# Optimization experiments

Measured on AMD Instinct MI355X. Metric: run time of the kernel, lower is better.

The kernel has to match this reference:

```python
import jax, jax.numpy as jnp
import numpy as np

HEADS = 4
SCALE = 10.0
DIM = 128
VOL = (16, 16, 16)
BATCH = 2
EPS = 1e-12  # F.normalize eps


def setup_inputs() -> dict:
    key = jax.random.key(0)
    ks = jax.random.split(key, 7)
    h, w, z = VOL
    shape = (BATCH, DIM, h, w, z)
    wstd = 1.0 / np.sqrt(DIM)
    return {
        "x": jax.random.normal(ks[0], shape, dtype=jnp.float32),
        "cond_x": jax.random.normal(ks[1], shape, dtype=jnp.float32),
        "Wq": jax.random.normal(ks[2], (DIM, DIM), dtype=jnp.float32) * wstd,
        "bq": jnp.zeros((DIM,), dtype=jnp.float32),
        "Wk": jax.random.normal(ks[3], (DIM, DIM), dtype=jnp.float32) * wstd,
        "bk": jnp.zeros((DIM,), dtype=jnp.float32),
        "Wv": jax.random.normal(ks[4], (DIM, DIM), dtype=jnp.float32) * wstd,
        "bv": jnp.zeros((DIM,), dtype=jnp.float32),
        "Wo": jax.random.normal(ks[5], (DIM, DIM), dtype=jnp.float32) * wstd,
        "bo": jnp.zeros((DIM,), dtype=jnp.float32),
    }


def _l2norm_last(t):
    # F.normalize(t, dim=-1): divide by max(||t||_2, eps) along last axis
    n = jnp.sqrt(jnp.sum(t * t, axis=-1, keepdims=True))
    return t / jnp.maximum(n, EPS)


def reference(x, cond_x, Wq, bq, Wk, bk, Wv, bv, Wo, bo):
    b, c, h, w, z = x.shape
    N = h * w * z
    d = c // HEADS
    xf = x.reshape(b, c, N)          # conv1x1 == per-voxel linear over channels
    cf = cond_x.reshape(b, c, N)
    q = jnp.einsum('oc,bcn->bon', Wq, xf) + bq[None, :, None]
    k = jnp.einsum('oc,bcn->bon', Wk, cf) + bk[None, :, None]
    v = jnp.einsum('oc,bcn->bon', Wv, cf) + bv[None, :, None]
    # 'b (h c) n -> b h c n'
    q = q.reshape(b, HEADS, d, N)
    k = k.reshape(b, HEADS, d, N)
    v = v.reshape(b, HEADS, d, N)
    # NOTE: original normalizes dim=-1 of [b,h,d,N] -> over the SPATIAL axis
    q = _l2norm_last(q)
    k = _l2norm_last(k)
    sim = jnp.einsum('bhdi,bhdj->bhij', q, k) * SCALE   # [b,h,N,N]
    attn = jax.nn.softmax(sim, axis=-1)
    out = jnp.einsum('bhij,bhdj->bhid', attn, v)        # [b,h,N,d]
    # 'b h n d -> b (h d) n' then back to volume
    out = out.transpose(0, 1, 3, 2).reshape(b, c, N)
    out = jnp.einsum('oc,bcn->bon', Wo, out) + bo[None, :, None]
    return out.reshape(b, c, h, w, z)
```

## Files before the change

kernel.cpp:

```cpp
#include <hip/hip_runtime.h>
#include <hip/hip_bf16.h>
#include <math.h>

#define NSP 4096
#define CD 128
#define NB 2
#define NH 4
#define JS 4
#define JSTEP 64
#define NSTEP ((NSP / JS) / JSTEP)

typedef __attribute__((ext_vector_type(8))) short bf16x8;
typedef __attribute__((ext_vector_type(4))) float f32x4;

static constexpr float QSCALE = 10.0f * 1.4426950408889634f;

__device__ __forceinline__ ushort f2bf(float f) {
    union { float f; unsigned u; } v; v.f = f;
    unsigned r = v.u + 0x7fffu + ((v.u >> 16) & 1u);
    return (ushort)(r >> 16);
}
__device__ __forceinline__ float bf2f(ushort u) {
    union { unsigned u; float f; } v; v.u = ((unsigned)u) << 16;
    return v.f;
}
__device__ __forceinline__ unsigned pk2bf(float a, float b) {
    union { __hip_bfloat162 h; unsigned u; } t;
    t.h = __float22bfloat162_rn(make_float2(a, b));
    return t.u;
}
__device__ __forceinline__ void gload_lds16(const void* g, void* l) {
    __builtin_amdgcn_global_load_lds(
        (const __attribute__((address_space(1))) unsigned int*)g,
        (__attribute__((address_space(3))) unsigned int*)l, 16, 0, 0);
}

__global__ __launch_bounds__(256) void cast_all(
    const float* __restrict__ x, const float* __restrict__ cx,
    const float* __restrict__ Wq, const float* __restrict__ Wk,
    const float* __restrict__ Wv, const float* __restrict__ Wo,
    ushort* __restrict__ Xt, ushort* __restrict__ Ct, ushort* __restrict__ Wall)
{
    const int t = threadIdx.x;
    if (blockIdx.x >= 128) {
        const int sub = blockIdx.x - 128;
        const int m = blockIdx.z * 2 + blockIdx.y;
        const float* src = (m == 0) ? Wq : (m == 1) ? Wk : (m == 2) ? Wv : Wo;
        const int off = sub * 1024 + t * 4;
        const float4 v = *(const float4*)(src + off);
        ushort4 o;
        o.x = f2bf(v.x); o.y = f2bf(v.y); o.z = f2bf(v.z); o.w = f2bf(v.w);
        *(ushort4*)(Wall + m * 16384 + off) = o;
        return;
    }
    __shared__ ushort L[32][130];
    const int n0 = blockIdx.x * 32;
    const int b  = blockIdx.y;
    const float* in = (blockIdx.z == 0) ? x : cx;
    ushort* outp    = (blockIdx.z == 0) ? Xt : Ct;
    const int nl = t & 31, cq = t >> 5;
    #pragma unroll
    for (int cc = cq; cc < CD; cc += 8)
        L[nl][cc] = f2bf(in[((size_t)b * CD + cc) * NSP + n0 + nl]);
    __syncthreads();
    const int nr = t >> 3, cs = (t & 7) * 16;
    unsigned u[8];
    #pragma unroll
    for (int w = 0; w < 8; ++w)
        u[w] = (unsigned)L[nr][cs + 2 * w] | ((unsigned)L[nr][cs + 2 * w + 1] << 16);
    ushort* dst = outp + ((size_t)(b * NSP + n0 + nr)) * CD + cs;
    *(uint4*)(dst)     = make_uint4(u[0], u[1], u[2], u[3]);
    *(uint4*)(dst + 8) = make_uint4(u[4], u[5], u[6], u[7]);
}

__global__ __launch_bounds__(256) void proj_qkv_mfma(
    const ushort* __restrict__ Xt, const ushort* __restrict__ Ct,
    const ushort* __restrict__ Wall,
    const float* __restrict__ Bq, const float* __restrict__ Bk, const float* __restrict__ Bv,
    ushort* __restrict__ Qt, ushort* __restrict__ Kt, ushort* __restrict__ V16,
    float* __restrict__ partQ, float* __restrict__ partK)
{
    const int t = threadIdx.x;
    const int wid = t >> 6, lane = t & 63;
    const int g = lane >> 4, n16 = lane & 15;
    const int nt = blockIdx.x;
    const int b  = nt >> 8;
    const int xblk = nt & 255;
    const int nb = xblk * 16;

    const size_t xrow = ((size_t)(b * NSP + nb + n16)) * CD;
    bf16x8 bx[4], bc[4];
    #pragma unroll
    for (int ks = 0; ks < 4; ++ks) {
        bx[ks] = *(const bf16x8*)(Xt + xrow + ks * 32 + g * 8);
        bc[ks] = *(const bf16x8*)(Ct + xrow + ks * 32 + g * 8);
    }
    const int jb = nb >> 6, jr = (nb & 63) + n16;

    #pragma unroll
    for (int hf = 0; hf < 2; ++hf) {
        const int o0 = hf * 64 + wid * 16;
        const ushort* Wq = Wall          + (size_t)(o0 + n16) * CD;
        const ushort* Wk = Wall + 16384  + (size_t)(o0 + n16) * CD;
        const ushort* Wv = Wall + 32768  + (size_t)(o0 + n16) * CD;

        f32x4 aq = {0,0,0,0}, ak = {0,0,0,0}, av = {0,0,0,0};
        #pragma unroll
        for (int ks = 0; ks < 4; ++ks) {
            const int k0 = ks * 32 + g * 8;
            const bf16x8 wqf = *(const bf16x8*)(Wq + k0);
            const bf16x8 wkf = *(const bf16x8*)(Wk + k0);
            const bf16x8 wvf = *(const bf16x8*)(Wv + k0);
            aq = __builtin_amdgcn_mfma_f32_16x16x32_bf16(wqf, bx[ks], aq, 0, 0, 0);
            ak = __builtin_amdgcn_mfma_f32_16x16x32_bf16(wkf, bc[ks], ak, 0, 0, 0);
            av = __builtin_amdgcn_mfma_f32_16x16x32_bf16(wvf, bc[ks], av, 0, 0, 0);
        }
        float qv[4], kv[4], sq[4], sk[4];
        #pragma unroll
        for (int r = 0; r < 4; ++r) {
            const int o = o0 + 4 * g + r;
            qv[r] = aq[r] + Bq[o];
            kv[r] = ak[r] + Bk[o];
            V16[((size_t)(b * CD + o)) * NSP + nb + n16] = f2bf(av[r] + Bv[o]);
            sq[r] = qv[r] * qv[r]; sk[r] = kv[r] * kv[r];
        }
        {
            const int o_first = o0 + 4 * g;
            const int bh = b * NH + (o_first >> 5);
            const int chunk = ((o_first & 31) >> 3);
            const size_t idx = (((size_t)(bh * 64 + jb)) * 4 + chunk) * 512
                             + (size_t)jr * 8 + 4 * (g & 1);
            uint2 qs, ks2;
            qs.x  = pk2bf(qv[0], qv[1]); qs.y  = pk2bf(qv[2], qv[3]);
            ks2.x = pk2bf(kv[0], kv[1]); ks2.y = pk2bf(kv[2], kv[3]);
            *(uint2*)(Qt + idx) = qs;
            *(uint2*)(Kt + idx) = ks2;
        }
        #pragma unroll
        for (int r = 0; r < 4; ++r) {
            #pragma unroll
            for (int off = 1; off < 16; off <<= 1) {
                sq[r] += __shfl_xor(sq[r], off);
                sk[r] += __shfl_xor(sk[r], off);
            }
        }
        if (n16 == 0) {
            #pragma unroll
            for (int r = 0; r < 4; ++r) {
                const int ch = b * CD + o0 + 4 * g + r;
                partQ[(size_t)ch * 256 + xblk] = sq[r];
                partK[(size_t)ch * 256 + xblk] = sk[r];
            }
        }
    }
}

__global__ __launch_bounds__(256) void normfin(
    const float* __restrict__ partQ, const float* __restrict__ partK,
    float* __restrict__ fsc)
{
    const int ch = blockIdx.x;
    const int t = threadIdx.x;
    float vq = partQ[(size_t)ch * 256 + t];
    float vk = partK[(size_t)ch * 256 + t];
    #pragma unroll
    for (int off = 32; off > 0; off >>= 1) {
        vq += __shfl_down(vq, off, 64);
        vk += __shfl_down(vk, off, 64);
    }
    __shared__ float redq[4], redk[4];
    if ((t & 63) == 0) { redq[t >> 6] = vq; redk[t >> 6] = vk; }
    __syncthreads();
    if (t == 0) {
        const float nq = sqrtf(redq[0] + redq[1] + redq[2] + redq[3]);
        const float nk = sqrtf(redk[0] + redk[1] + redk[2] + redk[3]);
        fsc[ch] = QSCALE / (fmaxf(nq, 1e-12f) * fmaxf(nk, 1e-12f));
    }
}

__global__ __launch_bounds__(256, 4) void attn_mfma(
    const ushort* __restrict__ Qt, const ushort* __restrict__ Kt,
    const ushort* __restrict__ V16, const float* __restrict__ fsc,
    unsigned* __restrict__ pacc, float* __restrict__ pl)
{
    __shared__ __align__(16) ushort Kl[4][2048];
    __shared__ __align__(16) ushort Vl[4][2048];

    const int t = threadIdx.x;
    const int wid = t >> 6, lane = t & 63;
    const int g = lane >> 4, n16 = lane & 15;
    const int f = blockIdx.x;
    const int bh = f & 7, it32 = (f >> 3) & 31, js = f >> 8;
    const int b = bh >> 2, h = bh & 3;
    const int i0 = it32 * 128 + wid * 32;

    const ushort* QtB = Qt + (size_t)bh * NSP * 32;
    const ushort* KtB = Kt + (size_t)bh * NSP * 32;
    const ushort* Vb  = V16 + (size_t)(b * CD + h * 32) * NSP;

    const float* fb = fsc + b * CD + h * 32 + g * 8;
    const f32x4 fA = *(const f32x4*)(fb);
    const f32x4 fB = *(const f32x4*)(fb + 4);

    const size_t qoff = ((size_t)(i0 >> 6) * 4 + g) * 512 + (size_t)(i0 & 63) * 8;
    const bf16x8 qr0 = *(const bf16x8*)(QtB + qoff + n16 * 8);
    const bf16x8 qr1 = *(const bf16x8*)(QtB + qoff + (16 + n16) * 8);
    auto scaleq = [&](bf16x8 q) -> bf16x8 {
        union { unsigned u[4]; bf16x8 v; } o;
        o.u[0] = pk2bf(bf2f((ushort)q[0]) * fA.x, bf2f((ushort)q[1]) * fA.y);
        o.u[1] = pk2bf(bf2f((ushort)q[2]) * fA.z, bf2f((ushort)q[3]) * fA.w);
        o.u[2] = pk2bf(bf2f((ushort)q[4]) * fB.x, bf2f((ushort)q[5]) * fB.y);
        o.u[3] = pk2bf(bf2f((ushort)q[6]) * fB.z, bf2f((ushort)q[7]) * fB.w);
        return o.v;
    };
    const bf16x8 qf[2] = { scaleq(qr0), scaleq(qr1) };

    f32x4 acc[2][2] = {{{0,0,0,0},{0,0,0,0}},{{0,0,0,0},{0,0,0,0}}};
    float l0 = 0.f, l1 = 0.f;
    const f32x4 zero = {0,0,0,0};

    const int klp = lane ^ (wid * 2);
    const int vd  = wid * 8 + (lane >> 3);
    const int vsw = (lane & 7) ^ (lane >> 3);
    auto stageK = [&](int buf, int jt) {
        gload_lds16(KtB + ((size_t)(jt >> 6) * 4 + wid) * 512 + klp * 8,
                    &Kl[buf][wid * 512]);
    };
    auto stageV = [&](int buf, int jt) {
        gload_lds16(Vb + (size_t)vd * NSP + jt + vsw * 8, &Vl[buf][wid * 512]);
    };

    const int jbeg = js * (NSP / JS);
    stageK(0, jbeg);          stageV(0, jbeg);
    stageK(1, jbeg + JSTEP);  stageV(1, jbeg + JSTEP);

    for (int step = 0; step < NSTEP; ++step) {
        const int jt = jbeg + step * JSTEP;
        if (step + 2 < NSTEP) {
            stageK((step + 2) & 3, jt + 2 * JSTEP);
            stageV((step + 2) & 3, jt + 2 * JSTEP);
            asm volatile("s_waitcnt vmcnt(4)" ::: "memory");
        } else if (step + 1 < NSTEP) {
            asm volatile("s_waitcnt vmcnt(2)" ::: "memory");
        } else {
            asm volatile("s_waitcnt vmcnt(0)" ::: "memory");
        }
        __builtin_amdgcn_s_barrier();
        const int cur = step & 3;
        __builtin_amdgcn_s_setprio(1);

        bf16x8 kf[2][2];
        union { uint2 u2[2]; bf16x8 v; } vf[2][2];
        #pragma unroll
        for (int s = 0; s < 2; ++s) {
            kf[s][0] = *(const bf16x8*)(&Kl[cur][g * 512 + ((s * 32 + n16) ^ (g * 2)) * 8]);
            kf[s][1] = *(const bf16x8*)(&Kl[cur][g * 512 + ((s * 32 + 16 + n16) ^ (g * 2)) * 8]);
            const int c0 = ((4 * s + (g >> 1)) ^ (n16 & 7)) * 8 + (g & 1) * 4;
            const int c1 = ((4 * s + 2 + (g >> 1)) ^ (n16 & 7)) * 8 + (g & 1) * 4;
            vf[s][0].u2[0] = *(const uint2*)(&Vl[cur][n16 * 64 + c0]);
            vf[s][0].u2[1] = *(const uint2*)(&Vl[cur][n16 * 64 + c1]);
            vf[s][1].u2[0] = *(const uint2*)(&Vl[cur][(16 + n16) * 64 + c0]);
            vf[s][1].u2[1] = *(const uint2*)(&Vl[cur][(16 + n16) * 64 + c1]);
        }
        f32x4 sv[2][2][2];
        #pragma unroll
        for (int s = 0; s < 2; ++s)
            #pragma unroll
            for (int it = 0; it < 2; ++it) {
                sv[s][it][0] = __builtin_amdgcn_mfma_f32_16x16x32_bf16(kf[s][0], qf[it], zero, 0, 0, 0);
                sv[s][it][1] = __builtin_amdgcn_mfma_f32_16x16x32_bf16(kf[s][1], qf[it], zero, 0, 0, 0);
            }

        union { unsigned u[4]; bf16x8 v; } pf[2][2];
        #pragma unroll
        for (int s = 0; s < 2; ++s)
            #pragma unroll
            for (int it = 0; it < 2; ++it) {
                const f32x4 s0 = sv[s][it][0], s1 = sv[s][it][1];
                const float p0 = __builtin_amdgcn_exp2f(s0.x);
                const float p1 = __builtin_amdgcn_exp2f(s0.y);
                const float p2 = __builtin_amdgcn_exp2f(s0.z);
                const float p3 = __builtin_amdgcn_exp2f(s0.w);
                const float p4 = __builtin_amdgcn_exp2f(s1.x);
                const float p5 = __builtin_amdgcn_exp2f(s1.y);
                const float p6 = __builtin_amdgcn_exp2f(s1.z);
                const float p7 = __builtin_amdgcn_exp2f(s1.w);
                const float ps = ((p0 + p1) + (p2 + p3)) + ((p4 + p5) + (p6 + p7));
                if (it) l1 += ps; else l0 += ps;
                pf[s][it].u[0] = pk2bf(p0, p1);
                pf[s][it].u[1] = pk2bf(p2, p3);
                pf[s][it].u[2] = pk2bf(p4, p5);
                pf[s][it].u[3] = pk2bf(p6, p7);
            }

        #pragma unroll
        for (int s = 0; s < 2; ++s)
            #pragma unroll
            for (int it = 0; it < 2; ++it) {
                acc[it][0] = __builtin_amdgcn_mfma_f32_16x16x32_bf16(vf[s][0].v, pf[s][it].v, acc[it][0], 0, 0, 0);
                acc[it][1] = __builtin_amdgcn_mfma_f32_16x16x32_bf16(vf[s][1].v, pf[s][it].v, acc[it][1], 0, 0, 0);
            }
        __builtin_amdgcn_s_setprio(0);
    }

    l0 += __shfl_xor(l0, 16); l0 += __shfl_xor(l0, 32);
    l1 += __shfl_xor(l1, 16); l1 += __shfl_xor(l1, 32);

    const size_t base = (size_t)js * 8 + bh;
    if (lane < 16) {
        pl[base * NSP + i0 + n16]      = l0;
        pl[base * NSP + i0 + 16 + n16] = l1;
    }
    unsigned* pb = pacc + base * 16 * NSP;
    const int col0 = i0 + n16, col1 = i0 + 16 + n16;
    pb[(size_t)(2 * g)     * NSP + col0] = pk2bf(acc[0][0][0], acc[0][0][1]);
    pb[(size_t)(2 * g + 1) * NSP + col0] = pk2bf(acc[0][0][2], acc[0][0][3]);
    pb[(size_t)(8 + 2 * g)     * NSP + col0] = pk2bf(acc[0][1][0], acc[0][1][1]);
    pb[(size_t)(8 + 2 * g + 1) * NSP + col0] = pk2bf(acc[0][1][2], acc[0][1][3]);
    pb[(size_t)(2 * g)     * NSP + col1] = pk2bf(acc[1][0][0], acc[1][0][1]);
    pb[(size_t)(2 * g + 1) * NSP + col1] = pk2bf(acc[1][0][2], acc[1][0][3]);
    pb[(size_t)(8 + 2 * g)     * NSP + col1] = pk2bf(acc[1][1][0], acc[1][1][1]);
    pb[(size_t)(8 + 2 * g + 1) * NSP + col1] = pk2bf(acc[1][1][2], acc[1][1][3]);
}

__global__ __launch_bounds__(256) void combine_proj_out(
    const unsigned* __restrict__ pacc, const float* __restrict__ pl,
    const ushort* __restrict__ Wall, const float* __restrict__ Bo,
    float* __restrict__ outp)
{
    __shared__ __align__(16) ushort Yl[16][128];
    const int t = threadIdx.x;
    const int nt = blockIdx.x;
    const int b  = nt >> 8;
    const int nb = (nt & 255) * 16;

    {
        const int nl = t & 15, hh = (t >> 4) & 3, q = t >> 6;
        const int bh = b * NH + hh;
        const int n = nb + nl;
        float L = 0.f;
        #pragma unroll
        for (int s = 0; s < JS; ++s) L += pl[((size_t)(s * 8 + bh)) * NSP + n];
        const float invL = 1.0f / L;
        unsigned u[4];
        #pragma unroll
        for (int e = 0; e < 4; ++e) {
            const int dp = q * 4 + e;
            float a0 = 0.f, a1 = 0.f;
            #pragma unroll
            for (int s = 0; s < JS; ++s) {
                const unsigned w = pacc[(((size_t)(s * 8 + bh)) * 16 + dp) * NSP + n];
                union { unsigned u; float f; } lo, hi;
                lo.u = w << 16; hi.u = w & 0xffff0000u;
                a0 += lo.f; a1 += hi.f;
            }
            u[e] = pk2bf(a0 * invL, a1 * invL);
        }
        const int chunk = hh * 4 + q;
        *(uint4*)(&Yl[nl][((chunk ^ (nl & 7)) * 8)]) = make_uint4(u[0], u[1], u[2], u[3]);
    }
    __syncthreads();

    const int wid = t >> 6, lane = t & 63;
    const int g = lane >> 4, n16 = lane & 15;
    const ushort* Wo = Wall + 49152;
    #pragma unroll
    for (int half = 0; half < 2; ++half) {
        const int o0 = half * 64 + wid * 16;
        const size_t wrow = (size_t)(o0 + n16) * CD;
        f32x4 a = {0,0,0,0};
        #pragma unroll
        for (int ks = 0; ks < 4; ++ks) {
            const bf16x8 wf = *(const bf16x8*)(Wo + wrow + ks * 32 + g * 8);
            const int chunk = ks * 4 + g;
            const bf16x8 yf = *(const bf16x8*)(&Yl[n16][((chunk ^ (n16 & 7)) * 8)]);
            a = __builtin_amdgcn_mfma_f32_16x16x32_bf16(wf, yf, a, 0, 0, 0);
        }
        #pragma unroll
        for (int r = 0; r < 4; ++r) {
            const int o = o0 + 4 * g + r;
            outp[((size_t)(b * CD + o)) * NSP + nb + n16] = a[r] + Bo[o];
        }
    }
}

extern "C" void kernel_launch(void* const* d_in, const int* in_sizes, int n_in,
                              void* d_out, int out_size, void* d_ws, size_t ws_size,
                              hipStream_t stream)
{
    const float* x  = (const float*)d_in[0];
    const float* cx = (const float*)d_in[1];
    const float* Wq = (const float*)d_in[2];
    const float* bq = (const float*)d_in[3];
    const float* Wk = (const float*)d_in[4];
    const float* bk = (const float*)d_in[5];
    const float* Wv = (const float*)d_in[6];
    const float* bv = (const float*)d_in[7];
    const float* Wo = (const float*)d_in[8];
    const float* bo = (const float*)d_in[9];
    float* out = (float*)d_out;

    char* w = (char*)d_ws;
    float*   fsc  = (float*)w;   w += 4096;
    float*   partQ = (float*)w;  w += (size_t)NB * CD * 256 * 4;
    float*   partK = (float*)w;  w += (size_t)NB * CD * 256 * 4;
    ushort*  Qt   = (ushort*)w;  w += (size_t)NB * NH * NSP * 32 * 2;
    ushort*  Kt   = (ushort*)w;  w += (size_t)NB * NH * NSP * 32 * 2;
    ushort*  V16  = (ushort*)w;  w += (size_t)NB * CD * NSP * 2;
    unsigned* pacc = (unsigned*)w; w += (size_t)JS * 8 * 16 * NSP * 4;
    float*   pl   = (float*)w;   w += (size_t)JS * 8 * NSP * 4;
    ushort*  Xt   = (ushort*)w;  w += (size_t)NB * NSP * CD * 2;
    ushort*  Ct   = (ushort*)w;  w += (size_t)NB * NSP * CD * 2;
    ushort*  Wall = (ushort*)w;

    cast_all<<<dim3(144, NB, 2), 256, 0, stream>>>(x, cx, Wq, Wk, Wv, Wo, Xt, Ct, Wall);
    proj_qkv_mfma<<<dim3(512), 256, 0, stream>>>(Xt, Ct, Wall, bq, bk, bv,
                                                 Qt, Kt, V16, partQ, partK);
    normfin<<<dim3(256), 256, 0, stream>>>(partQ, partK, fsc);
    attn_mfma<<<dim3(1024), 256, 0, stream>>>(Qt, Kt, V16, fsc, pacc, pl);
    combine_proj_out<<<dim3(512), 256, 0, stream>>>(pacc, pl, Wall, bo, out);
}
```

Measured before the change: 61.97 us.

## Fuse fp32-to-bf16 cast into projection kernels and drop cast_all launch

Removes the separate cast_all kernel. The QKV projection now loads fp32 x and cond_x directly, converts them to bf16 into swizzled shared-memory tiles, and converts weights to bf16 on the fly from fp32. The output projection also converts Wo on the fly. This eliminates one launch and the round trip of the bf16 intermediates through global memory, at the cost of reading weights redundantly in fp32 (twice the bytes) and doing per-block conversion work.

```diff
diff --git a/kernel.cpp b/kernel.cpp
--- a/kernel.cpp
+++ b/kernel.cpp
@@ -34,52 +34,26 @@
         (const __attribute__((address_space(1))) unsigned int*)g,
         (__attribute__((address_space(3))) unsigned int*)l, 16, 0, 0);
 }
-
-__global__ __launch_bounds__(256) void cast_all(
+__device__ __forceinline__ bf16x8 wfrag(const float* p) {
+    const float4 a = *(const float4*)(p);
+    const float4 b = *(const float4*)(p + 4);
+    union { unsigned u[4]; bf16x8 v; } o;
+    o.u[0] = pk2bf(a.x, a.y);
+    o.u[1] = pk2bf(a.z, a.w);
+    o.u[2] = pk2bf(b.x, b.y);
+    o.u[3] = pk2bf(b.z, b.w);
+    return o.v;
+}
+
+__global__ __launch_bounds__(256) void proj_qkv_mfma(
     const float* __restrict__ x, const float* __restrict__ cx,
-    const float* __restrict__ Wq, const float* __restrict__ Wk,
-    const float* __restrict__ Wv, const float* __restrict__ Wo,
-    ushort* __restrict__ Xt, ushort* __restrict__ Ct, ushort* __restrict__ Wall)
-{
-    const int t = threadIdx.x;
-    if (blockIdx.x >= 128) {
-        const int sub = blockIdx.x - 128;
-        const int m = blockIdx.z * 2 + blockIdx.y;
-        const float* src = (m == 0) ? Wq : (m == 1) ? Wk : (m == 2) ? Wv : Wo;
-        const int off = sub * 1024 + t * 4;
-        const float4 v = *(const float4*)(src + off);
-        ushort4 o;
-        o.x = f2bf(v.x); o.y = f2bf(v.y); o.z = f2bf(v.z); o.w = f2bf(v.w);
-        *(ushort4*)(Wall + m * 16384 + off) = o;
-        return;
-    }
-    __shared__ ushort L[32][130];
-    const int n0 = blockIdx.x * 32;
-    const int b  = blockIdx.y;
-    const float* in = (blockIdx.z == 0) ? x : cx;
-    ushort* outp    = (blockIdx.z == 0) ? Xt : Ct;
-    const int nl = t & 31, cq = t >> 5;
-    #pragma unroll
-    for (int cc = cq; cc < CD; cc += 8)
-        L[nl][cc] = f2bf(in[((size_t)b * CD + cc) * NSP + n0 + nl]);
-    __syncthreads();
-    const int nr = t >> 3, cs = (t & 7) * 16;
-    unsigned u[8];
-    #pragma unroll
-    for (int w = 0; w < 8; ++w)
-        u[w] = (unsigned)L[nr][cs + 2 * w] | ((unsigned)L[nr][cs + 2 * w + 1] << 16);
-    ushort* dst = outp + ((size_t)(b * NSP + n0 + nr)) * CD + cs;
-    *(uint4*)(dst)     = make_uint4(u[0], u[1], u[2], u[3]);
-    *(uint4*)(dst + 8) = make_uint4(u[4], u[5], u[6], u[7]);
-}
-
-__global__ __launch_bounds__(256) void proj_qkv_mfma(
-    const ushort* __restrict__ Xt, const ushort* __restrict__ Ct,
-    const ushort* __restrict__ Wall,
+    const float* __restrict__ WqF, const float* __restrict__ WkF, const float* __restrict__ WvF,
     const float* __restrict__ Bq, const float* __restrict__ Bk, const float* __restrict__ Bv,
     ushort* __restrict__ Qt, ushort* __restrict__ Kt, ushort* __restrict__ V16,
     float* __restrict__ partQ, float* __restrict__ partK)
 {
+    __shared__ __align__(16) ushort Xl[16][128];
+    __shared__ __align__(16) ushort Cl[16][128];
     const int t = threadIdx.x;
     const int wid = t >> 6, lane = t & 63;
     const int g = lane >> 4, n16 = lane & 15;
@@ -88,29 +62,47 @@
     const int xblk = nt & 255;
     const int nb = xblk * 16;
 
-    const size_t xrow = ((size_t)(b * NSP + nb + n16)) * CD;
+    {
+        const int c = t >> 1, half = t & 1;
+        const float* xs = x  + ((size_t)b * CD + c) * NSP + nb + half * 8;
+        const float* cs = cx + ((size_t)b * CD + c) * NSP + nb + half * 8;
+        float xv[8], cv[8];
+        *(float4*)(xv)     = *(const float4*)(xs);
+        *(float4*)(xv + 4) = *(const float4*)(xs + 4);
+        *(float4*)(cv)     = *(const float4*)(cs);
+        *(float4*)(cv + 4) = *(const float4*)(cs + 4);
+        const int c8 = c >> 3, ce = c & 7;
+        #pragma unroll
+        for (int j = 0; j < 8; ++j) {
+            const int n = half * 8 + j;
+            const int col = ((c8 ^ (n & 7)) << 3) + ce;
+            Xl[n][col] = f2bf(xv[j]);
+            Cl[n][col] = f2bf(cv[j]);
+        }
+    }
+    __syncthreads();
+
     bf16x8 bx[4], bc[4];
     #pragma unroll
     for (int ks = 0; ks < 4; ++ks) {
-        bx[ks] = *(const bf16x8*)(Xt + xrow + ks * 32 + g * 8);
-        bc[ks] = *(const bf16x8*)(Ct + xrow + ks * 32 + g * 8);
+        const int col = (((4 * ks + g) ^ (n16 & 7)) << 3);
+        bx[ks] = *(const bf16x8*)(&Xl[n16][col]);
+        bc[ks] = *(const bf16x8*)(&Cl[n16][col]);
     }
     const int jb = nb >> 6, jr = (nb & 63) + n16;
 
     #pragma unroll
     for (int hf = 0; hf < 2; ++hf) {
         const int o0 = hf * 64 + wid * 16;
-        const ushort* Wq = Wall          + (size_t)(o0 + n16) * CD;
-        const ushort* Wk = Wall + 16384  + (size_t)(o0 + n16) * CD;
-        const ushort* Wv = Wall + 32768  + (size_t)(o0 + n16) * CD;
+        const size_t wrow = (size_t)(o0 + n16) * CD;
 
         f32x4 aq = {0,0,0,0}, ak = {0,0,0,0}, av = {0,0,0,0};
         #pragma unroll
         for (int ks = 0; ks < 4; ++ks) {
             const int k0 = ks * 32 + g * 8;
-            const bf16x8 wqf = *(const bf16x8*)(Wq + k0);
-            const bf16x8 wkf = *(const bf16x8*)(Wk + k0);
-            const bf16x8 wvf = *(const bf16x8*)(Wv + k0);
+            const bf16x8 wqf = wfrag(WqF + wrow + k0);
+            const bf16x8 wkf = wfrag(WkF + wrow + k0);
+            const bf16x8 wvf = wfrag(WvF + wrow + k0);
             aq = __builtin_amdgcn_mfma_f32_16x16x32_bf16(wqf, bx[ks], aq, 0, 0, 0);
             ak = __builtin_amdgcn_mfma_f32_16x16x32_bf16(wkf, bc[ks], ak, 0, 0, 0);
             av = __builtin_amdgcn_mfma_f32_16x16x32_bf16(wvf, bc[ks], av, 0, 0, 0);
@@ -325,7 +317,7 @@
 
 __global__ __launch_bounds__(256) void combine_proj_out(
     const unsigned* __restrict__ pacc, const float* __restrict__ pl,
-    const ushort* __restrict__ Wall, const float* __restrict__ Bo,
+    const float* __restrict__ WoF, const float* __restrict__ Bo,
     float* __restrict__ outp)
 {
     __shared__ __align__(16) ushort Yl[16][128];
@@ -363,7 +355,6 @@
 
     const int wid = t >> 6, lane = t & 63;
     const int g = lane >> 4, n16 = lane & 15;
-    const ushort* Wo = Wall + 49152;
     #pragma unroll
     for (int half = 0; half < 2; ++half) {
         const int o0 = half * 64 + wid * 16;
@@ -371,7 +362,7 @@
         f32x4 a = {0,0,0,0};
         #pragma unroll
         for (int ks = 0; ks < 4; ++ks) {
-            const bf16x8 wf = *(const bf16x8*)(Wo + wrow + ks * 32 + g * 8);
+            const bf16x8 wf = wfrag(WoF + wrow + ks * 32 + g * 8);
             const int chunk = ks * 4 + g;
             const bf16x8 yf = *(const bf16x8*)(&Yl[n16][((chunk ^ (n16 & 7)) * 8)]);
             a = __builtin_amdgcn_mfma_f32_16x16x32_bf16(wf, yf, a, 0, 0, 0);
@@ -408,15 +399,11 @@
     ushort*  Kt   = (ushort*)w;  w += (size_t)NB * NH * NSP * 32 * 2;
     ushort*  V16  = (ushort*)w;  w += (size_t)NB * CD * NSP * 2;
     unsigned* pacc = (unsigned*)w; w += (size_t)JS * 8 * 16 * NSP * 4;
-    float*   pl   = (float*)w;   w += (size_t)JS * 8 * NSP * 4;
-    ushort*  Xt   = (ushort*)w;  w += (size_t)NB * NSP * CD * 2;
-    ushort*  Ct   = (ushort*)w;  w += (size_t)NB * NSP * CD * 2;
-    ushort*  Wall = (ushort*)w;
-
-    cast_all<<<dim3(144, NB, 2), 256, 0, stream>>>(x, cx, Wq, Wk, Wv, Wo, Xt, Ct, Wall);
-    proj_qkv_mfma<<<dim3(512), 256, 0, stream>>>(Xt, Ct, Wall, bq, bk, bv,
+    float*   pl   = (float*)w;
+
+    proj_qkv_mfma<<<dim3(512), 256, 0, stream>>>(x, cx, Wq, Wk, Wv, bq, bk, bv,
                                                  Qt, Kt, V16, partQ, partK);
     normfin<<<dim3(256), 256, 0, stream>>>(partQ, partK, fsc);
     attn_mfma<<<dim3(1024), 256, 0, stream>>>(Qt, Kt, V16, fsc, pacc, pl);
-    combine_proj_out<<<dim3(512), 256, 0, stream>>>(pacc, pl, Wall, bo, out);
-}
+    combine_proj_out<<<dim3(512), 256, 0, stream>>>(pacc, pl, Wo, bo, out);
+}
```

New measurement: 63.27 us. 1.02x slower.
